# Performance work log

Hardware: AMD Instinct MI355X
Metric: run time of the kernel (lower is better)

## Reference

```python
import jax, jax.numpy as jnp
import numpy as np


def setup_inputs() -> dict:
    key = jax.random.key(0)
    k1, k2, k3 = jax.random.split(key, 3)
    B, S, E = 4, 4096, 512
    x = jax.random.normal(k1, (B, S, E), dtype=jnp.float32)
    # xavier_uniform for Linear weights; zero biases (per _reset_parameters)
    lim_qkv = float(np.sqrt(6.0 / (E + 3 * E)))
    W_qkv = jax.random.uniform(k2, (3 * E, E), minval=-lim_qkv, maxval=lim_qkv, dtype=jnp.float32)
    b_qkv = jnp.zeros((3 * E,), dtype=jnp.float32)
    lim_out = float(np.sqrt(6.0 / (E + E)))
    W_out = jax.random.uniform(k3, (E, E), minval=-lim_out, maxval=lim_out, dtype=jnp.float32)
    b_out = jnp.zeros((E,), dtype=jnp.float32)
    return {"x": x, "W_qkv": W_qkv, "b_qkv": b_qkv, "W_out": W_out, "b_out": b_out}


def reference(x, W_qkv, b_qkv, W_out, b_out):
    B, S, E = x.shape
    H = 8
    D = E // H
    qkv = x @ W_qkv.T + b_qkv                      # [B,S,3E]
    qkv = qkv.reshape(B, S, H, 3 * D)
    q, k, v = jnp.split(qkv, 3, axis=-1)            # each [B,S,H,D]
    q = jax.nn.sigmoid(q)
    k = jax.nn.sigmoid(k)
    # flow conservation normalizers (sum over seq dim=1, then feature dim=3)
    i = jnp.sum(q * jnp.sum(k, axis=1, keepdims=True), axis=3, keepdims=True)      # [B,S,H,1]
    o = jnp.sum(k * jnp.sum(q, axis=1, keepdims=True), axis=3, keepdims=True)
    i_hat = jnp.sum(q * jnp.sum(k / o, axis=1, keepdims=True), axis=3, keepdims=True)
    o_hat = jnp.sum(k * jnp.sum(q / i, axis=1, keepdims=True), axis=3, keepdims=True)
    # NOTE: faithful to source — matmul batches over (B,S) and contracts the HEAD axis
    vw = v * jax.nn.softmax(o_hat, axis=1)          # [B,S,H,D]
    kv = jnp.einsum('bshd,bshe->bsde', k, vw)       # [B,S,D,D]
    r = jnp.einsum('bshd,bsde->bshe', q / i, kv) * jax.nn.sigmoid(i_hat)  # [B,S,H,D]
    values = r.reshape(B, S, E)
    return values @ W_out.T + b_out
```

## Files before the change

### kernel.cpp

```cpp
#include <hip/hip_runtime.h>
#include <cstdint>
#include <cstddef>

#define B_ 4
#define S_ 4096
#define E_ 512
#define NPOS 16384
#define QKVC 1536
#define K_ 512

typedef unsigned short u16;
typedef u16    u16x8  __attribute__((ext_vector_type(8)));
typedef u16    u16x4  __attribute__((ext_vector_type(4)));
typedef __bf16 bf16x8 __attribute__((ext_vector_type(8)));
typedef float  f32x4  __attribute__((ext_vector_type(4)));

__device__ __forceinline__ u16 f2bf(float f) {
    unsigned u = __builtin_bit_cast(unsigned, f);
    unsigned r = (u + 0x7fffu + ((u >> 16) & 1u)) >> 16;
    return (u16)r;
}
__device__ __forceinline__ float bf2f(u16 u) {
    return __builtin_bit_cast(float, (unsigned)u << 16);
}
__device__ __forceinline__ float rcpf(float x) { return __builtin_amdgcn_rcpf(x); }

__device__ __forceinline__ void async16(const void* g, void* lds) {
    __builtin_amdgcn_global_load_lds(
        (const __attribute__((address_space(1))) unsigned int*)g,
        (__attribute__((address_space(3))) unsigned int*)lds, 16, 0, 0);
}

__global__ void cvt_kernel(const float4* __restrict__ in, u16x4* __restrict__ out, int n4) {
    int i = blockIdx.x * 256 + threadIdx.x;
    if (i < n4) {
        float4 v = in[i];
        u16x4 o;
        o[0] = f2bf(v.x); o[1] = f2bf(v.y); o[2] = f2bf(v.z); o[3] = f2bf(v.w);
        out[i] = o;
    }
}

__global__ __launch_bounds__(256) void gemm_qkv(
        const u16* __restrict__ A, const u16* __restrict__ Bw,
        const float* __restrict__ bias,
        u16* __restrict__ Qb, u16* __restrict__ Kb, u16* __restrict__ Vb,
        int K) {
    __shared__ u16 As[128 * 32];
    __shared__ u16 Bs[128 * 32];
    const int tid  = threadIdx.x;
    const int wave = tid >> 6, lane = tid & 63;
    const int m0 = blockIdx.y * 128, n0 = blockIdx.x * 128;
    const int wm = (wave & 1) * 64, wn = (wave >> 1) * 64;

    const int srow = wave * 16 + (lane >> 2);
    const int scol = (lane & 3) * 8;
    const u16* Ap = A  + (size_t)(m0 + srow) * K + scol;
    const u16* Bp = Bw + (size_t)(n0 + srow) * K + scol;
    u16* AsW = &As[wave * 512];
    u16* BsW = &Bs[wave * 512];
    const size_t rstep = (size_t)64 * K;

    f32x4 acc[4][4] = {};
    const int fr = lane & 15, fk = (lane >> 4) * 8;

    for (int k0 = 0; k0 < K; k0 += 32) {
        async16(Ap + k0,         AsW);
        async16(Ap + k0 + rstep, AsW + 2048);
        async16(Bp + k0,         BsW);
        async16(Bp + k0 + rstep, BsW + 2048);
        __syncthreads();
        bf16x8 a[4], b[4];
        #pragma unroll
        for (int i = 0; i < 4; ++i)
            a[i] = *(const bf16x8*)&As[(wm + i * 16 + fr) * 32 + fk];
        #pragma unroll
        for (int j = 0; j < 4; ++j)
            b[j] = *(const bf16x8*)&Bs[(wn + j * 16 + fr) * 32 + fk];
        #pragma unroll
        for (int i = 0; i < 4; ++i)
            #pragma unroll
            for (int j = 0; j < 4; ++j)
                acc[i][j] = __builtin_amdgcn_mfma_f32_16x16x32_bf16(a[i], b[j], acc[i][j], 0, 0, 0);
        __syncthreads();
    }

    const int cn = lane & 15, rb = (lane >> 4) * 4;
    const int cg   = (n0 + wn) >> 6;
    const int type = cg % 3;
    const int hb   = cg / 3;
    u16* dst = (type == 0) ? Qb : (type == 1) ? Kb : Vb;
    const bool sg = (type < 2);
    #pragma unroll
    for (int i = 0; i < 4; ++i) {
        int mbase = m0 + wm + i * 16 + rb;
        #pragma unroll
        for (int j = 0; j < 4; ++j) {
            int ccol = j * 16 + cn;
            float bv = bias[n0 + wn + ccol];
            int outcol = hb * 64 + ccol;
            f32x4 av = acc[i][j];
            #pragma unroll
            for (int r = 0; r < 4; ++r) {
                float v = av[r] + bv;
                if (sg) v = 1.f / (1.f + __expf(-v));
                dst[(size_t)(mbase + r) * 512 + outcol] = f2bf(v);
            }
        }
    }
}

__global__ __launch_bounds__(256) void gemm_out(
        const u16* __restrict__ A, const u16* __restrict__ Bw,
        const float* __restrict__ bias, float* __restrict__ C,
        int N, int K) {
    __shared__ u16 As[128 * 32];
    __shared__ u16 Bs[128 * 32];
    const int tid  = threadIdx.x;
    const int wave = tid >> 6, lane = tid & 63;
    const int m0 = blockIdx.y * 128, n0 = blockIdx.x * 128;
    const int wm = (wave & 1) * 64, wn = (wave >> 1) * 64;
    const int srow = wave * 16 + (lane >> 2);
    const int scol = (lane & 3) * 8;
    const u16* Ap = A  + (size_t)(m0 + srow) * K + scol;
    const u16* Bp = Bw + (size_t)(n0 + srow) * K + scol;
    u16* AsW = &As[wave * 512];
    u16* BsW = &Bs[wave * 512];
    const size_t rstep = (size_t)64 * K;
    f32x4 acc[4][4] = {};
    const int fr = lane & 15, fk = (lane >> 4) * 8;
    for (int k0 = 0; k0 < K; k0 += 32) {
        async16(Ap + k0,         AsW);
        async16(Ap + k0 + rstep, AsW + 2048);
        async16(Bp + k0,         BsW);
        async16(Bp + k0 + rstep, BsW + 2048);
        __syncthreads();
        bf16x8 a[4], b[4];
        #pragma unroll
        for (int i = 0; i < 4; ++i)
            a[i] = *(const bf16x8*)&As[(wm + i * 16 + fr) * 32 + fk];
        #pragma unroll
        for (int j = 0; j < 4; ++j)
            b[j] = *(const bf16x8*)&Bs[(wn + j * 16 + fr) * 32 + fk];
        #pragma unroll
        for (int i = 0; i < 4; ++i)
            #pragma unroll
            for (int j = 0; j < 4; ++j)
                acc[i][j] = __builtin_amdgcn_mfma_f32_16x16x32_bf16(a[i], b[j], acc[i][j], 0, 0, 0);
        __syncthreads();
    }
    const int cn = lane & 15, rb = (lane >> 4) * 4;
    #pragma unroll
    for (int i = 0; i < 4; ++i) {
        int mbase = m0 + wm + i * 16 + rb;
        #pragma unroll
        for (int j = 0; j < 4; ++j) {
            int nn = n0 + wn + j * 16 + cn;
            float bv = bias[nn];
            f32x4 av = acc[i][j];
            #pragma unroll
            for (int r = 0; r < 4; ++r)
                C[(size_t)(mbase + r) * N + nn] = av[r] + bv;
        }
    }
}

__global__ __launch_bounds__(256) void sum_qk(const u16* __restrict__ Qg, const u16* __restrict__ Kg,
                                              float* __restrict__ sumq, float* __restrict__ sumk) {
    int b = blockIdx.x, sc = blockIdx.y;
    int w = threadIdx.x >> 6, lane = threadIdx.x & 63;
    float aq[8] = {}, ak[8] = {};
    int p0 = b * S_ + sc * 32 + w * 8;
    for (int it = 0; it < 8; ++it) {
        size_t off = (size_t)(p0 + it) * 512 + lane * 8;
        u16x8 q8 = *(const u16x8*)(Qg + off);
        u16x8 k8 = *(const u16x8*)(Kg + off);
        #pragma unroll
        for (int j = 0; j < 8; ++j) { aq[j] += bf2f(q8[j]); ak[j] += bf2f(k8[j]); }
    }
    __shared__ float red[4][1024];
    #pragma unroll
    for (int j = 0; j < 8; ++j) {
        red[w][lane * 8 + j]       = aq[j];
        red[w][512 + lane * 8 + j] = ak[j];
    }
    __syncthreads();
    int t = threadIdx.x;
    #pragma unroll
    for (int rr = 0; rr < 4; ++rr) {
        int slot = rr * 256 + t;
        float s = red[0][slot] + red[1][slot] + red[2][slot] + red[3][slot];
        float* dst = (slot < 512) ? &sumq[b * 512 + slot] : &sumk[b * 512 + (slot - 512)];
        atomicAdd(dst, s);
    }
}

__global__ __launch_bounds__(256) void fused_io(const u16* __restrict__ Qg, const u16* __restrict__ Kg,
                                                const float* __restrict__ sumq, const float* __restrict__ sumk,
                                                float* __restrict__ iv,
                                                float* __restrict__ sumqi, float* __restrict__ sumko) {
    int b = blockIdx.x, sc = blockIdx.y;
    int w = threadIdx.x >> 6, lane = threadIdx.x & 63;
    float skL[8], sqL[8];
    #pragma unroll
    for (int j = 0; j < 8; ++j) {
        skL[j] = sumk[b * 512 + lane * 8 + j];
        sqL[j] = sumq[b * 512 + lane * 8 + j];
    }
    float aqi[8] = {}, ako[8] = {};
    int p0 = b * S_ + sc * 32 + w * 8;
    for (int it = 0; it < 8; ++it) {
        int p = p0 + it;
        size_t off = (size_t)p * 512 + lane * 8;
        u16x8 q8 = *(const u16x8*)(Qg + off);
        u16x8 k8 = *(const u16x8*)(Kg + off);
        float qf[8], kf[8];
        #pragma unroll
        for (int j = 0; j < 8; ++j) { qf[j] = bf2f(q8[j]); kf[j] = bf2f(k8[j]); }
        float di = 0.f, dox = 0.f;
        #pragma unroll
        for (int j = 0; j < 8; ++j) { di += qf[j] * skL[j]; dox += kf[j] * sqL[j]; }
        di  += __shfl_xor(di, 1);  di  += __shfl_xor(di, 2);  di  += __shfl_xor(di, 4);
        dox += __shfl_xor(dox, 1); dox += __shfl_xor(dox, 2); dox += __shfl_xor(dox, 4);
        if ((lane & 7) == 0) iv[(size_t)p * 8 + (lane >> 3)] = di;
        float ri = rcpf(di), ro = rcpf(dox);
        #pragma unroll
        for (int j = 0; j < 8; ++j) { aqi[j] += qf[j] * ri; ako[j] += kf[j] * ro; }
    }
    __shared__ float red[4][1024];
    #pragma unroll
    for (int j = 0; j < 8; ++j) {
        red[w][lane * 8 + j]       = aqi[j];
        red[w][512 + lane * 8 + j] = ako[j];
    }
    __syncthreads();
    int t = threadIdx.x;
    #pragma unroll
    for (int rr = 0; rr < 4; ++rr) {
        int slot = rr * 256 + t;
        float s = red[0][slot] + red[1][slot] + red[2][slot] + red[3][slot];
        float* dst = (slot < 512) ? &sumqi[b * 512 + slot] : &sumko[b * 512 + (slot - 512)];
        atomicAdd(dst, s);
    }
}

__global__ __launch_bounds__(256) void io2_kernel(const u16* __restrict__ Qg, const u16* __restrict__ Kg,
                                                  const float* __restrict__ sumqi, const float* __restrict__ sumko,
                                                  const float* __restrict__ iv,
                                                  float* __restrict__ rowsc, float* __restrict__ wexp,
                                                  float* __restrict__ sm) {
    int b = blockIdx.x, sc = blockIdx.y;
    int w = threadIdx.x >> 6, lane = threadIdx.x & 63;
    float skoL[8], sqiL[8];
    #pragma unroll
    for (int j = 0; j < 8; ++j) {
        skoL[j] = sumko[b * 512 + lane * 8 + j];
        sqiL[j] = sumqi[b * 512 + lane * 8 + j];
    }
    float smacc = 0.f;
    int p0 = b * S_ + sc * 32 + w * 8;
    for (int it = 0; it < 8; ++it) {
        int p = p0 + it;
        size_t off = (size_t)p * 512 + lane * 8;
        u16x8 q8 = *(const u16x8*)(Qg + off);
        u16x8 k8 = *(const u16x8*)(Kg + off);
        float dih = 0.f, doh = 0.f;
        #pragma unroll
        for (int j = 0; j < 8; ++j) {
            dih += bf2f(q8[j]) * skoL[j];
            doh += bf2f(k8[j]) * sqiL[j];
        }
        dih += __shfl_xor(dih, 1); dih += __shfl_xor(dih, 2); dih += __shfl_xor(dih, 4);
        doh += __shfl_xor(doh, 1); doh += __shfl_xor(doh, 2); doh += __shfl_xor(doh, 4);
        if ((lane & 7) == 0) {
            int h = lane >> 3;
            float sig = 1.f / (1.f + __expf(-dih));
            rowsc[(size_t)p * 8 + h] = sig * rcpf(iv[(size_t)p * 8 + h]);
            float we = __expf(fminf(doh, 80.f));
            wexp[(size_t)p * 8 + h] = we;
            smacc += we;
        }
    }
    __shared__ float sr[4][8];
    if ((lane & 7) == 0) sr[w][lane >> 3] = smacc;
    __syncthreads();
    if (threadIdx.x < 8)
        atomicAdd(&sm[b * 8 + threadIdx.x],
                  sr[0][threadIdx.x] + sr[1][threadIdx.x] + sr[2][threadIdx.x] + sr[3][threadIdx.x]);
}

__global__ __launch_bounds__(256) void finalize_kernel(
        const u16* __restrict__ Qg, const u16* __restrict__ Kg, const u16* __restrict__ Vg,
        const float* __restrict__ rowsc, const float* __restrict__ wexp, const float* __restrict__ sm,
        u16* __restrict__ Rg) {
    __shared__ float Ml[4][2][8][9];
    __shared__ float vw[4][2][8][68];
    int w = threadIdx.x >> 6, lane = threadIdx.x & 63;
    int p0 = (blockIdx.x * 4 + w) * 2;
    int b = p0 >> 12;

    {
        int pl = (lane >> 3) & 1, hh = lane & 7, quad = lane >> 4;
        const u16* qa = Qg + (size_t)(p0 + pl) * 512 + hh * 64 + quad * 8;
        const u16* ka = Kg + (size_t)(p0 + pl) * 512 + hh * 64 + quad * 8;
        bf16x8 a0 = __builtin_bit_cast(bf16x8, *(const u16x8*)qa);
        bf16x8 a1 = __builtin_bit_cast(bf16x8, *(const u16x8*)(qa + 32));
        bf16x8 b0 = __builtin_bit_cast(bf16x8, *(const u16x8*)ka);
        bf16x8 b1 = __builtin_bit_cast(bf16x8, *(const u16x8*)(ka + 32));
        f32x4 accm = {0.f, 0.f, 0.f, 0.f};
        accm = __builtin_amdgcn_mfma_f32_16x16x32_bf16(a0, b0, accm, 0, 0, 0);
        accm = __builtin_amdgcn_mfma_f32_16x16x32_bf16(a1, b1, accm, 0, 0, 0);
        if (((lane >> 5) & 1) == ((lane >> 3) & 1)) {
            int plm = lane >> 5, hr = ((lane >> 4) & 1) * 4, h2 = lane & 7;
            #pragma unroll
            for (int r = 0; r < 4; ++r) Ml[w][plm][hr + r][h2] = accm[r];
        }
    }
    {
        int hv = lane >> 3, e0 = (lane & 7) * 8;
        float invsm = rcpf(sm[b * 8 + hv]);
        #pragma unroll
        for (int pl = 0; pl < 2; ++pl) {
            u16x8 v8 = *(const u16x8*)(Vg + (size_t)(p0 + pl) * 512 + lane * 8);
            float wgt = wexp[(size_t)(p0 + pl) * 8 + hv] * invsm;
            f32x4 x0, x1;
            #pragma unroll
            for (int j = 0; j < 4; ++j) { x0[j] = bf2f(v8[j]) * wgt; x1[j] = bf2f(v8[4 + j]) * wgt; }
            *(f32x4*)&vw[w][pl][hv][e0]     = x0;
            *(f32x4*)&vw[w][pl][hv][e0 + 4] = x1;
        }
    }
    __syncthreads();
    {
        int pl = lane >> 5, idx = lane & 31, h = idx >> 2, eq = (idx & 3) * 16;
        float out[16] = {};
        #pragma unroll
        for (int h2 = 0; h2 < 8; ++h2) {
            float m = Ml[w][pl][h][h2];
            #pragma unroll
            for (int c = 0; c < 4; ++c) {
                f32x4 vv = *(const f32x4*)&vw[w][pl][h2][eq + c * 4];
                #pragma unroll
                for (int j = 0; j < 4; ++j) out[c * 4 + j] += m * vv[j];
            }
        }
        float rs = rowsc[(size_t)(p0 + pl) * 8 + h];
        u16x8 o0, o1;
        #pragma unroll
        for (int j = 0; j < 8; ++j) { o0[j] = f2bf(out[j] * rs); o1[j] = f2bf(out[8 + j] * rs); }
        u16* dst = Rg + (size_t)(p0 + pl) * 512 + h * 64 + eq;
        *(u16x8*)dst       = o0;
        *(u16x8*)(dst + 8) = o1;
    }
}

extern "C" void kernel_launch(void* const* d_in, const int* in_sizes, int n_in,
                              void* d_out, int out_size, void* d_ws, size_t ws_size,
                              hipStream_t stream) {
    const float* x    = (const float*)d_in[0];
    const float* Wqkv = (const float*)d_in[1];
    const float* bqkv = (const float*)d_in[2];
    const float* Wout = (const float*)d_in[3];
    const float* bout = (const float*)d_in[4];
    float* out = (float*)d_out;
    char* ws = (char*)d_ws;

    constexpr size_t SZ_XBF  = (size_t)NPOS * E_ * 2;
    constexpr size_t SZ_WQBF = (size_t)QKVC * E_ * 2;
    constexpr size_t SZ_WOBF = (size_t)E_ * E_ * 2;
    constexpr size_t SZ_QKVB = (size_t)NPOS * E_ * 2;
    constexpr size_t SZ_SUM  = (size_t)B_ * 512 * 4;
    constexpr size_t SZ_V8   = (size_t)NPOS * 8 * 4;

    size_t off = 0;
    u16*   xbf   = (u16*)(ws + off);   off += SZ_XBF;
    u16*   wqbf  = (u16*)(ws + off);   off += SZ_WQBF;
    u16*   wobf  = (u16*)(ws + off);   off += SZ_WOBF;
    u16*   Qb    = (u16*)(ws + off);   off += SZ_QKVB;
    u16*   Kb    = (u16*)(ws + off);   off += SZ_QKVB;
    u16*   Vb    = (u16*)(ws + off);   off += SZ_QKVB;
    char*  zbase = ws + off;
    float* sumq  = (float*)(ws + off); off += SZ_SUM;
    float* sumk  = (float*)(ws + off); off += SZ_SUM;
    float* sumqi = (float*)(ws + off); off += SZ_SUM;
    float* sumko = (float*)(ws + off); off += SZ_SUM;
    float* sm    = (float*)(ws + off); off += 256;
    size_t zlen  = (char*)(ws + off) - zbase;
    float* iv    = (float*)(ws + off); off += SZ_V8;
    float* rowsc = (float*)(ws + off); off += SZ_V8;
    float* wexp  = (float*)(ws + off); off += SZ_V8;
    u16*   rbf   = xbf;

    hipMemsetAsync(zbase, 0, zlen, stream);

    cvt_kernel<<<(NPOS * E_ / 4) / 256, 256, 0, stream>>>((const float4*)x, (u16x4*)xbf, NPOS * E_ / 4);
    cvt_kernel<<<(QKVC * E_ / 4) / 256, 256, 0, stream>>>((const float4*)Wqkv, (u16x4*)wqbf, QKVC * E_ / 4);
    cvt_kernel<<<(E_ * E_ / 4) / 256, 256, 0, stream>>>((const float4*)Wout, (u16x4*)wobf, E_ * E_ / 4);

    gemm_qkv<<<dim3(QKVC / 128, NPOS / 128), 256, 0, stream>>>(xbf, wqbf, bqkv, Qb, Kb, Vb, K_);

    sum_qk<<<dim3(B_, 128), 256, 0, stream>>>(Qb, Kb, sumq, sumk);
    fused_io<<<dim3(B_, 128), 256, 0, stream>>>(Qb, Kb, sumq, sumk, iv, sumqi, sumko);
    io2_kernel<<<dim3(B_, 128), 256, 0, stream>>>(Qb, Kb, sumqi, sumko, iv, rowsc, wexp, sm);
    finalize_kernel<<<NPOS / 8, 256, 0, stream>>>(Qb, Kb, Vb, rowsc, wexp, sm, rbf);

    gemm_out<<<dim3(E_ / 128, NPOS / 128), 256, 0, stream>>>(rbf, wobf, bout, out, E_, K_);
}
```

Measured before the change: 198.9 us.

## Double-buffer LDS tiles, XOR-swizzle layout, and raise MFMA priority in GEMMs

Both GEMM kernels now keep two LDS buffers, so the async global-to-LDS load of the next K tile is issued before the MFMAs on the current tile, with one barrier per iteration instead of two. The 16-byte column chunk each lane writes and reads is XOR-swizzled by row to reduce LDS bank conflicts on the fragment reads. The MFMA block is also wrapped in s_setprio to favour the matrix work. The cost is double the LDS per block, which may lower occupancy. Correctness with a single barrier depends on the global_load_lds writes having completed by that barrier.

```diff
diff --git a/kernel.cpp b/kernel.cpp
--- a/kernel.cpp
+++ b/kernel.cpp
@@ -41,49 +41,66 @@
     }
 }
 
+__device__ __forceinline__ void mfma_step(const u16* AsB, const u16* BsB,
+                                          int wm, int wn, int fr, int fkk,
+                                          f32x4 (&acc)[4][4]) {
+    bf16x8 a[4], b[4];
+    #pragma unroll
+    for (int i = 0; i < 4; ++i)
+        a[i] = *(const bf16x8*)&AsB[(wm + i * 16 + fr) * 32 + fkk];
+    #pragma unroll
+    for (int j = 0; j < 4; ++j)
+        b[j] = *(const bf16x8*)&BsB[(wn + j * 16 + fr) * 32 + fkk];
+    __builtin_amdgcn_s_setprio(1);
+    #pragma unroll
+    for (int i = 0; i < 4; ++i)
+        #pragma unroll
+        for (int j = 0; j < 4; ++j)
+            acc[i][j] = __builtin_amdgcn_mfma_f32_16x16x32_bf16(a[i], b[j], acc[i][j], 0, 0, 0);
+    __builtin_amdgcn_s_setprio(0);
+}
+
 __global__ __launch_bounds__(256) void gemm_qkv(
         const u16* __restrict__ A, const u16* __restrict__ Bw,
         const float* __restrict__ bias,
         u16* __restrict__ Qb, u16* __restrict__ Kb, u16* __restrict__ Vb,
         int K) {
-    __shared__ u16 As[128 * 32];
-    __shared__ u16 Bs[128 * 32];
+    __shared__ u16 As[2][128 * 32];
+    __shared__ u16 Bs[2][128 * 32];
     const int tid  = threadIdx.x;
     const int wave = tid >> 6, lane = tid & 63;
     const int m0 = blockIdx.y * 128, n0 = blockIdx.x * 128;
     const int wm = (wave & 1) * 64, wn = (wave >> 1) * 64;
 
     const int srow = wave * 16 + (lane >> 2);
-    const int scol = (lane & 3) * 8;
-    const u16* Ap = A  + (size_t)(m0 + srow) * K + scol;
-    const u16* Bp = Bw + (size_t)(n0 + srow) * K + scol;
-    u16* AsW = &As[wave * 512];
-    u16* BsW = &Bs[wave * 512];
+    const int cgs  = (lane & 3) ^ ((lane >> 2) & 3) ^ ((lane >> 4) & 3);
+    const u16* Ap = A  + (size_t)(m0 + srow) * K + cgs * 8;
+    const u16* Bp = Bw + (size_t)(n0 + srow) * K + cgs * 8;
+    const int woff = wave * 512;
     const size_t rstep = (size_t)64 * K;
 
     f32x4 acc[4][4] = {};
-    const int fr = lane & 15, fk = (lane >> 4) * 8;
-
-    for (int k0 = 0; k0 < K; k0 += 32) {
-        async16(Ap + k0,         AsW);
-        async16(Ap + k0 + rstep, AsW + 2048);
-        async16(Bp + k0,         BsW);
-        async16(Bp + k0 + rstep, BsW + 2048);
+    const int fr  = lane & 15;
+    const int fkk = (((lane >> 4) ^ (fr & 3) ^ ((fr >> 2) & 3))) * 8;
+
+    async16(Ap,         &As[0][woff]);
+    async16(Ap + rstep, &As[0][woff + 2048]);
+    async16(Bp,         &Bs[0][woff]);
+    async16(Bp + rstep, &Bs[0][woff + 2048]);
+    __syncthreads();
+
+    int cur = 0;
+    for (int k0 = 32; k0 < K; k0 += 32) {
+        const int nxt = cur ^ 1;
+        async16(Ap + k0,         &As[nxt][woff]);
+        async16(Ap + k0 + rstep, &As[nxt][woff + 2048]);
+        async16(Bp + k0,         &Bs[nxt][woff]);
+        async16(Bp + k0 + rstep, &Bs[nxt][woff + 2048]);
+        mfma_step(As[cur], Bs[cur], wm, wn, fr, fkk, acc);
         __syncthreads();
-        bf16x8 a[4], b[4];
-        #pragma unroll
-        for (int i = 0; i < 4; ++i)
-            a[i] = *(const bf16x8*)&As[(wm + i * 16 + fr) * 32 + fk];
-        #pragma unroll
-        for (int j = 0; j < 4; ++j)
-            b[j] = *(const bf16x8*)&Bs[(wn + j * 16 + fr) * 32 + fk];
-        #pragma unroll
-        for (int i = 0; i < 4; ++i)
-            #pragma unroll
-            for (int j = 0; j < 4; ++j)
-                acc[i][j] = __builtin_amdgcn_mfma_f32_16x16x32_bf16(a[i], b[j], acc[i][j], 0, 0, 0);
-        __syncthreads();
-    }
+        cur = nxt;
+    }
+    mfma_step(As[cur], Bs[cur], wm, wn, fr, fkk, acc);
 
     const int cn = lane & 15, rb = (lane >> 4) * 4;
     const int cg   = (n0 + wn) >> 6;
@@ -114,41 +131,41 @@
         const u16* __restrict__ A, const u16* __restrict__ Bw,
         const float* __restrict__ bias, float* __restrict__ C,
         int N, int K) {
-    __shared__ u16 As[128 * 32];
-    __shared__ u16 Bs[128 * 32];
+    __shared__ u16 As[2][128 * 32];
+    __shared__ u16 Bs[2][128 * 32];
     const int tid  = threadIdx.x;
     const int wave = tid >> 6, lane = tid & 63;
     const int m0 = blockIdx.y * 128, n0 = blockIdx.x * 128;
     const int wm = (wave & 1) * 64, wn = (wave >> 1) * 64;
     const int srow = wave * 16 + (lane >> 2);
-    const int scol = (lane & 3) * 8;
-    const u16* Ap = A  + (size_t)(m0 + srow) * K + scol;
-    const u16* Bp = Bw + (size_t)(n0 + srow) * K + scol;
-    u16* AsW = &As[wave * 512];
-    u16* BsW = &Bs[wave * 512];
+    const int cgs  = (lane & 3) ^ ((lane >> 2) & 3) ^ ((lane >> 4) & 3);
+    const u16* Ap = A  + (size_t)(m0 + srow) * K + cgs * 8;
+    const u16* Bp = Bw + (size_t)(n0 + srow) * K + cgs * 8;
+    const int woff = wave * 512;
     const size_t rstep = (size_t)64 * K;
     f32x4 acc[4][4] = {};
-    const int fr = lane & 15, fk = (lane >> 4) * 8;
-    for (int k0 = 0; k0 < K; k0 += 32) {
-        async16(Ap + k0,         AsW);
-        async16(Ap + k0 + rstep, AsW + 2048);
-        async16(Bp + k0,         BsW);
-        async16(Bp + k0 + rstep, BsW + 2048);
+    const int fr  = lane & 15;
+    const int fkk = (((lane >> 4) ^ (fr & 3) ^ ((fr >> 2) & 3))) * 8;
+
+    async16(Ap,         &As[0][woff]);
+    async16(Ap + rstep, &As[0][woff + 2048]);
+    async16(Bp,         &Bs[0][woff]);
+    async16(Bp + rstep, &Bs[0][woff + 2048]);
+    __syncthreads();
+
+    int cur = 0;
+    for (int k0 = 32; k0 < K; k0 += 32) {
+        const int nxt = cur ^ 1;
+        async16(Ap + k0,         &As[nxt][woff]);
+        async16(Ap + k0 + rstep, &As[nxt][woff + 2048]);
+        async16(Bp + k0,         &Bs[nxt][woff]);
+        async16(Bp + k0 + rstep, &Bs[nxt][woff + 2048]);
+        mfma_step(As[cur], Bs[cur], wm, wn, fr, fkk, acc);
         __syncthreads();
-        bf16x8 a[4], b[4];
-        #pragma unroll
-        for (int i = 0; i < 4; ++i)
-            a[i] = *(const bf16x8*)&As[(wm + i * 16 + fr) * 32 + fk];
-        #pragma unroll
-        for (int j = 0; j < 4; ++j)
-            b[j] = *(const bf16x8*)&Bs[(wn + j * 16 + fr) * 32 + fk];
-        #pragma unroll
-        for (int i = 0; i < 4; ++i)
-            #pragma unroll
-            for (int j = 0; j < 4; ++j)
-                acc[i][j] = __builtin_amdgcn_mfma_f32_16x16x32_bf16(a[i], b[j], acc[i][j], 0, 0, 0);
-        __syncthreads();
-    }
+        cur = nxt;
+    }
+    mfma_step(As[cur], Bs[cur], wm, wn, fr, fkk, acc);
+
     const int cn = lane & 15, rb = (lane >> 4) * 4;
     #pragma unroll
     for (int i = 0; i < 4; ++i) {
```

After: 200.8 us. Within noise of the previous version (+0.9%).
